# Kernel optimization log

Hardware: AMD Instinct MI355X
Metric: run time of the kernel (lower is better)

## Reference

```python
import jax, jax.numpy as jnp
import numpy as np

B, N, E_PER = 512, 256, 8192          # graphs, nodes per graph, edges per graph
FIN, H, K, FOUT = 128, 32, 16, 10     # in_channels, hidden, num clusters, out_channels
EPS = 1e-15


def setup_inputs() -> dict:
    key = jax.random.key(0)
    ks = jax.random.split(key, 12)
    x = jax.random.normal(ks[0], (B * N, FIN), jnp.float32)
    # intra-graph random edges, then offset into the global node index space
    src = jax.random.randint(ks[1], (B, E_PER), 0, N)
    dst = jax.random.randint(ks[2], (B, E_PER), 0, N)
    offs = (jnp.arange(B) * N)[:, None]
    edge_index = jnp.stack([(src + offs).reshape(-1), (dst + offs).reshape(-1)]).astype(jnp.int64)
    batch = jnp.repeat(jnp.arange(B), N).astype(jnp.int64)

    def lin(k, fin, fout):
        return (jax.random.normal(k, (fin, fout), jnp.float32) / np.sqrt(fin)).astype(jnp.float32)

    params = {
        'W_lin1': lin(ks[3], FIN, H), 'b_lin1': jnp.zeros((H,), jnp.float32),
        'W_rel1': lin(ks[4], H, H), 'b_rel1': jnp.zeros((H,), jnp.float32),
        'W_root1': lin(ks[5], H, H),
        'W_pool': lin(ks[6], H, K), 'b_pool': jnp.zeros((K,), jnp.float32),
        'W_rel2': lin(ks[7], H, H), 'b_rel2': jnp.zeros((H,), jnp.float32),
        'W_root2': lin(ks[8], H, H),
        'W_lin2': lin(ks[9], H, H), 'b_lin2': jnp.zeros((H,), jnp.float32),
        'W_lin3': lin(ks[10], H, FOUT), 'b_lin3': jnp.zeros((FOUT,), jnp.float32),
    }
    return {'x': x, 'edge_index': edge_index, 'batch': batch, **params}


def _densify(x, edge_index, batch):
    """to_dense_adj + to_dense_batch: [total,F] -> [B,N,F], [B,N,N], [B,N]."""
    n_total = x.shape[0]
    counts = jax.ops.segment_sum(jnp.ones((n_total,), jnp.int32), batch, num_segments=B)
    offsets = jnp.concatenate([jnp.zeros((1,), jnp.int32), jnp.cumsum(counts)[:-1]])
    pos = jnp.arange(n_total) - offsets[batch]            # position of node inside its graph
    eb = batch[edge_index[0]]                             # graph id of each edge
    adj = jnp.zeros((B, N, N), jnp.float32).at[eb, pos[edge_index[0]], pos[edge_index[1]]].add(1.0)
    xd = jnp.zeros((B, N, x.shape[1]), jnp.float32).at[batch, pos].set(x)
    mask = jnp.zeros((B, N), jnp.float32).at[batch, pos].set(1.0)
    return xd, adj, mask


def _dense_graph_conv(x, adj, W_rel, b_rel, W_root):
    # PyG DenseGraphConv(aggr='add'): lin_rel(adj @ x) + lin_root(x)
    return jnp.einsum('bnm,bmh,hk->bnk', adj, x, W_rel) + b_rel + x @ W_root


def _dense_mincut_pool(x, adj, s, mask):
    s = jax.nn.softmax(s, axis=-1)
    x = x * mask[..., None]
    s = s * mask[..., None]
    out = jnp.einsum('bnk,bnh->bkh', s, x)                        # s^T x
    out_adj = jnp.einsum('bnk,bnm,bmj->bkj', s, adj, s)           # s^T A s
    mincut_num = jnp.einsum('bkk->b', out_adj)
    d_flat = adj.sum(-1)                                          # degree
    mincut_den = jnp.einsum('bnk,bn,bnk->b', s, d_flat, s)        # trace(s^T D s)
    mincut_loss = jnp.mean(-(mincut_num / mincut_den))
    ss = jnp.einsum('bnk,bnj->bkj', s, s)
    ss_norm = jnp.linalg.norm(ss, axis=(-1, -2), keepdims=True)
    i_s = jnp.eye(K, dtype=jnp.float32)
    ortho_loss = jnp.mean(jnp.linalg.norm(ss / ss_norm - i_s / jnp.sqrt(jnp.float32(K)), axis=(-1, -2)))
    # zero diagonal, symmetric degree normalization
    diag_mask = 1.0 - i_s
    out_adj = out_adj * diag_mask
    d = jnp.sqrt(out_adj.sum(-1))[:, None, :] + EPS               # [B,1,K]
    out_adj = out_adj / d / jnp.swapaxes(d, 1, 2)
    return out, out_adj, mincut_loss, ortho_loss


def reference(x, edge_index, batch, W_lin1, b_lin1, W_rel1, b_rel1, W_root1,
              W_pool, b_pool, W_rel2, b_rel2, W_root2, W_lin2, b_lin2, W_lin3, b_lin3):
    xd, adj, mask = _densify(x, edge_index, batch)
    h = xd @ W_lin1 + b_lin1                                      # lin1
    h = _dense_graph_conv(h, adj, W_rel1, b_rel1, W_root1)        # conv1
    s2 = h @ W_pool + b_pool                                      # pool2
    h, adj_p, mincut_loss2, ortho_loss2 = _dense_mincut_pool(h, adj, s2, mask)
    h = _dense_graph_conv(h, adj_p, W_rel2, b_rel2, W_root2)      # conv2
    h = h.sum(axis=1)                                             # readout sum over clusters
    h = jax.nn.relu(h @ W_lin2 + b_lin2)
    h = h @ W_lin3 + b_lin3
    return jax.nn.log_softmax(h, axis=-1), mincut_loss2, ortho_loss2
```

## Files before the change

### kernel.cpp

```cpp
#include <hip/hip_runtime.h>

#define NB 512
#define NN 256
#define EPG 8192
#define FINC 128

typedef float f32x4 __attribute__((ext_vector_type(4)));
typedef short s16x8 __attribute__((ext_vector_type(8)));

__device__ __forceinline__ float bf2f(unsigned short u) {
  union { unsigned int i; float f; } x; x.i = ((unsigned int)u) << 16; return x.f;
}
__device__ __forceinline__ unsigned short f2bf(float f) {
  union { float f; unsigned int i; } x; x.f = f;
  unsigned int r = x.i + 0x7fffu + ((x.i >> 16) & 1u);
  return (unsigned short)(r >> 16);
}
__device__ __forceinline__ unsigned pk2(unsigned short a, unsigned short c) {
  return (unsigned)a | ((unsigned)c << 16);
}

union U16x8 { uint4 u; s16x8 s; };
__device__ __forceinline__ s16x8 dec8(unsigned d) {
  U16x8 o;
  o.u.x = 0x41804180u | ((d & 0x0000000Fu) << 3)  | ((d & 0x000000F0u) << 15);
  o.u.y = 0x41804180u | ((d & 0x00000F00u) >> 5)  | ((d & 0x0000F000u) << 7);
  o.u.z = 0x41804180u | ((d & 0x000F0000u) >> 13) | ((d & 0x00F00000u) >> 1);
  o.u.w = 0x41804180u | ((d & 0x0F000000u) >> 21) | ((d & 0xF0000000u) >> 9);
  return o.s;
}

struct Params {
  const void* x; const void* ei;
  const void *wl1, *bl1, *wr1, *br1, *wro1, *wp, *bp;
  const void *wr2, *br2, *wro2, *wl2, *bl2, *wl3, *bl3;
  float* out; float* ws;
};

__device__ __forceinline__ bool detect_bf16(const void* p) {
  const unsigned short* pw = (const unsigned short*)p;
  int sane = 0;
  for (int i = 0; i < 64; ++i) {
    unsigned e = (pw[i] >> 7) & 0xFFu;
    sane += (e > 96u && e < 132u) ? 1 : 0;
  }
  return sane >= 56;
}
__device__ __forceinline__ bool detect_i64(const void* p) {
  const int* pi = (const int*)p + EPG;
  int ok = 0;
  for (int i = 0; i < 32; ++i) ok += (pi[i] >= 256 && pi[i] < 512) ? 1 : 0;
  return ok < 24;
}
__device__ __forceinline__ float ldf(const void* p, int i, bool bf) {
  return bf ? bf2f(((const unsigned short*)p)[i]) : ((const float*)p)[i];
}

#define SMEM_TOTAL 81920

__global__ __launch_bounds__(1024, 8) void mincut_main(Params P) {
  extern __shared__ char smem[];
  const int t = threadIdx.x;
  const int b = blockIdx.x;

  int* flg = (int*)(smem + 78656);
  if (t == 0) {
    flg[0] = detect_bf16(P.wr1) ? 1 : 0;
    flg[1] = detect_i64(P.ei) ? 1 : 0;
  }
  __syncthreads();
  const bool BF  = (flg[0] != 0);
  const bool I64 = (flg[1] != 0);

  float* oadjb  = (float*)(smem + 2048);
  float* ddb    = (float*)(smem + 6144);
  float* caf    = (float*)(smem + 6208);
  float* psf    = (float*)(smem + 6272);
  float* qsf    = (float*)(smem + 6400);
  float* rb     = (float*)(smem + 8256);
  float* yb     = (float*)(smem + 8384);
  float* lgb    = (float*)(smem + 8512);
  float* rel2f  = (float*)(smem + 9216);
  float* root2f = (float*)(smem + 13312);
  float* lin2f  = (float*)(smem + 17408);
  float* lin3f  = (float*)(smem + 21504);
  float* brel2f = (float*)(smem + 22784);
  float* blin2f = (float*)(smem + 22912);
  float* blin3f = (float*)(smem + 23040);
  float* pbufH  = (float*)(smem + 24576);
  float* pbufL  = (float*)(smem + 26624);
  float* oadjH  = (float*)(smem + 28672);
  float* oadjL  = (float*)(smem + 29696);
  float* ssA    = (float*)(smem + 30720);
  float* ssX    = (float*)(smem + 31744);
  unsigned short* h0T  = (unsigned short*)(smem + 33792);
  unsigned short* h1Th = (unsigned short*)(smem + 33792);
  unsigned short* w1t  = (unsigned short*)(smem + 50688);
  unsigned short* zT   = (unsigned short*)(smem + 50688);
  unsigned short* sTh  = (unsigned short*)(smem + 50688);
  unsigned short* sTl  = (unsigned short*)(smem + 59136);
  unsigned short* wrelTh = (unsigned short*)(smem + 67584);
  unsigned short* wrelTl = (unsigned short*)(smem + 70144);
  unsigned short* wrootT = (unsigned short*)(smem + 72704);
  float* blin1f = (float*)(smem + 75264);
  unsigned short* taT = (unsigned short*)(smem + 67584);
  unsigned short* wpoolTh = (unsigned short*)(smem + 76032);
  unsigned short* wpoolTl = (unsigned short*)(smem + 77184);
  float*          colzF   = (float*)(smem + 78336);
  float*          colsF   = (float*)(smem + 78464);
  float*          scrE    = (float*)(smem + 78528);
  float*          bpf     = (float*)(smem + 78592);
  unsigned short* brel1h  = (unsigned short*)(smem + 81856);

  const int wv = t >> 6, lane = t & 63;
  const int lm = lane & 15, quad = lane >> 4;
  const int mbase = wv * 16;

  {
    uint4 z = {0u, 0u, 0u, 0u};
    for (int i = t; i < 2112; i += 1024) ((uint4*)smem)[i] = z;
  }
  if (t < 48) colzF[t] = 0.f;
  for (int e = t; e < 4096; e += 1024) {
    int k = e >> 5, c = e & 31;
    w1t[c * 136 + k] = f2bf(ldf(P.wl1, e, BF));
  }
  {
    int k = t >> 5, c = t & 31;
    float wr = ldf(P.wr1, t, BF);
    unsigned short hi = f2bf(wr);
    wrelTh[c * 40 + k] = hi;
    wrelTl[c * 40 + k] = f2bf(wr - bf2f(hi));
    wrootT[c * 40 + k] = f2bf(ldf(P.wro1, t, BF));
  }
  if (t < 512) {
    int m = t >> 4, c = t & 15;
    float w = ldf(P.wp, t, BF);
    unsigned short hi = f2bf(w);
    wpoolTh[c * 36 + m] = hi;
    wpoolTl[c * 36 + m] = f2bf(w - bf2f(hi));
  }
  if (t < 32) { blin1f[t] = ldf(P.bl1, t, BF); brel1h[t] = f2bf(ldf(P.br1, t, BF)); }
  if (t < 16) bpf[t] = ldf(P.bp, t, BF);
  __syncthreads();

  if (I64) {
    const uint4* s4 = (const uint4*)((const long long*)P.ei + (size_t)b * EPG) + t * 4;
    const uint4* d4 = (const uint4*)((const long long*)P.ei + (size_t)NB * EPG + (size_t)b * EPG) + t * 4;
    #pragma unroll
    for (int i = 0; i < 4; ++i) {
      uint4 a = s4[i], c = d4[i];
      unsigned n0 = (a.x & 255u) * 264u + (c.x & 255u);
      unsigned n1 = (a.z & 255u) * 264u + (c.z & 255u);
      atomicAdd((unsigned int*)(smem + ((n0 >> 3) << 2)), 1u << ((n0 & 7u) * 4u));
      atomicAdd((unsigned int*)(smem + ((n1 >> 3) << 2)), 1u << ((n1 & 7u) * 4u));
    }
  } else {
    const uint4* s4 = (const uint4*)((const int*)P.ei + (size_t)b * EPG) + t * 2;
    const uint4* d4 = (const uint4*)((const int*)P.ei + (size_t)NB * EPG + (size_t)b * EPG) + t * 2;
    #pragma unroll
    for (int i = 0; i < 2; ++i) {
      uint4 a = s4[i], c = d4[i];
      unsigned n0 = (a.x & 255u) * 264u + (c.x & 255u);
      unsigned n1 = (a.y & 255u) * 264u + (c.y & 255u);
      unsigned n2 = (a.z & 255u) * 264u + (c.z & 255u);
      unsigned n3 = (a.w & 255u) * 264u + (c.w & 255u);
      atomicAdd((unsigned int*)(smem + ((n0 >> 3) << 2)), 1u << ((n0 & 7u) * 4u));
      atomicAdd((unsigned int*)(smem + ((n1 >> 3) << 2)), 1u << ((n1 & 7u) * 4u));
      atomicAdd((unsigned int*)(smem + ((n2 >> 3) << 2)), 1u << ((n2 & 7u) * 4u));
      atomicAdd((unsigned int*)(smem + ((n3 >> 3) << 2)), 1u << ((n3 & 7u) * 4u));
    }
  }

  {
    f32x4 acc[2] = {{0.f,0.f,0.f,0.f},{0.f,0.f,0.f,0.f}};
    const size_t node = (size_t)(b * 256 + mbase + lm);
    #pragma unroll
    for (int ks = 0; ks < 4; ++ks) {
      const int k0 = ks * 32 + quad * 8;
      s16x8 a;
      if (BF) {
        a = *(const s16x8*)((const unsigned short*)P.x + node * 128 + k0);
      } else {
        const float* xp = (const float*)P.x + node * 128 + k0;
        f32x4 v0 = *(const f32x4*)xp;
        f32x4 v1 = *(const f32x4*)(xp + 4);
        #pragma unroll
        for (int j = 0; j < 4; ++j) { a[j] = (short)f2bf(v0[j]); a[4 + j] = (short)f2bf(v1[j]); }
      }
      #pragma unroll
      for (int ct = 0; ct < 2; ++ct) {
        s16x8 bh = *(const s16x8*)(w1t + (ct * 16 + lm) * 136 + k0);
        acc[ct] = __builtin_amdgcn_mfma_f32_16x16x32_bf16(a, bh, acc[ct], 0, 0, 0);
      }
    }
    #pragma unroll
    for (int ct = 0; ct < 2; ++ct) {
      const int c = ct * 16 + lm;
      float bias = blin1f[c];
      *(uint2*)(h0T + c * 264 + mbase + quad * 4) =
          make_uint2(pk2(f2bf(acc[ct][0] + bias), f2bf(acc[ct][1] + bias)),
                     pk2(f2bf(acc[ct][2] + bias), f2bf(acc[ct][3] + bias)));
    }
  }
  __syncthreads();

  f32x4 racc[2] = {{0.f,0.f,0.f,0.f},{0.f,0.f,0.f,0.f}};
  {
    s16x8 Ah;
    #pragma unroll
    for (int j = 0; j < 8; ++j) Ah[j] = (short)h0T[(quad * 8 + j) * 264 + mbase + lm];
    f32x4 zacc[2] = {{0.f,0.f,0.f,0.f},{0.f,0.f,0.f,0.f}};
    #pragma unroll
    for (int ct = 0; ct < 2; ++ct) {
      const int c = ct * 16 + lm;
      s16x8 brh = *(const s16x8*)(wrelTh + c * 40 + quad * 8);
      s16x8 brl = *(const s16x8*)(wrelTl + c * 40 + quad * 8);
      s16x8 bro = *(const s16x8*)(wrootT + c * 40 + quad * 8);
      zacc[ct] = __builtin_amdgcn_mfma_f32_16x16x32_bf16(Ah, brh, zacc[ct], 0, 0, 0);
      zacc[ct] = __builtin_amdgcn_mfma_f32_16x16x32_bf16(Ah, brl, zacc[ct], 0, 0, 0);
      racc[ct] = __builtin_amdgcn_mfma_f32_16x16x32_bf16(Ah, bro, racc[ct], 0, 0, 0);
    }
    #pragma unroll
    for (int ct = 0; ct < 2; ++ct) {
      unsigned short u0 = f2bf(zacc[ct][0]), u1 = f2bf(zacc[ct][1]);
      unsigned short u2 = f2bf(zacc[ct][2]), u3 = f2bf(zacc[ct][3]);
      *(uint2*)(zT + (ct * 16 + lm) * 264 + mbase + quad * 4) =
          make_uint2(pk2(u0, u1), pk2(u2, u3));
      float pz = (bf2f(u0) + bf2f(u1)) + (bf2f(u2) + bf2f(u3));
      pz += __shfl_xor(pz, 16, 64);
      pz += __shfl_xor(pz, 32, 64);
      if (lane < 16) atomicAdd(colzF + ct * 16 + lm, pz);
    }
  }
  __syncthreads();

  float degf;
  {
    f32x4 h1acc[2] = { racc[0], racc[1] };
    unsigned dsum = 0;
    const char* arow = smem + (mbase + lm) * 132;
    #pragma unroll
    for (int ks = 0; ks < 8; ++ks) {
      unsigned d = *(const unsigned int*)(arow + ks * 16 + quad * 4);
      unsigned v = (d & 0x0F0F0F0Fu) + ((d >> 4) & 0x0F0F0F0Fu);
      dsum += (v * 0x01010101u) >> 24;
      s16x8 af = dec8(d);
      const int v0 = ks * 32 + quad * 8;
      #pragma unroll
      for (int ct = 0; ct < 2; ++ct) {
        s16x8 bz = *(const s16x8*)(zT + (ct * 16 + lm) * 264 + v0);
        h1acc[ct] = __builtin_amdgcn_mfma_f32_16x16x32_bf16(af, bz, h1acc[ct], 0, 0, 0);
      }
    }
    dsum += __shfl_xor(dsum, 16, 64);
    dsum += __shfl_xor(dsum, 32, 64);
    degf = (float)dsum;
    #pragma unroll
    for (int ct = 0; ct < 2; ++ct) {
      const int c = ct * 16 + lm;
      float bias = bf2f(brel1h[c]) - 16.f * colzF[c];
      *(uint2*)(h1Th + c * 264 + mbase + quad * 4) =
          make_uint2(pk2(f2bf(h1acc[ct][0] + bias), f2bf(h1acc[ct][1] + bias)),
                     pk2(f2bf(h1acc[ct][2] + bias), f2bf(h1acc[ct][3] + bias)));
    }
  }
  __syncthreads();

  {
    s16x8 Ah1;
    #pragma unroll
    for (int j = 0; j < 8; ++j) Ah1[j] = (short)h1Th[(quad * 8 + j) * 264 + mbase + lm];
    s16x8 Bh, Bl;
    ((uint2*)&Bh)[0] = *(const uint2*)(wpoolTh + lm * 36 + quad * 8);
    ((uint2*)&Bh)[1] = *(const uint2*)(wpoolTh + lm * 36 + quad * 8 + 4);
    ((uint2*)&Bl)[0] = *(const uint2*)(wpoolTl + lm * 36 + quad * 8);
    ((uint2*)&Bl)[1] = *(const uint2*)(wpoolTl + lm * 36 + quad * 8 + 4);
    f32x4 lacc = {0.f, 0.f, 0.f, 0.f};
    lacc = __builtin_amdgcn_mfma_f32_16x16x32_bf16(Ah1, Bh, lacc, 0, 0, 0);
    lacc = __builtin_amdgcn_mfma_f32_16x16x32_bf16(Ah1, Bl, lacc, 0, 0, 0);
    f32x4 lg;
    float bm = bpf[lm];
    #pragma unroll
    for (int r = 0; r < 4; ++r) lg[r] = lacc[r] + bm;
    f32x4 mx = lg;
    #pragma unroll
    for (int m = 1; m <= 8; m <<= 1)
      #pragma unroll
      for (int r = 0; r < 4; ++r) mx[r] = fmaxf(mx[r], __shfl_xor(mx[r], m, 64));
    #pragma unroll
    for (int r = 0; r < 4; ++r) lg[r] = __expf(lg[r] - mx[r]);
    f32x4 sm = lg;
    #pragma unroll
    for (int m = 1; m <= 8; m <<= 1)
      #pragma unroll
      for (int r = 0; r < 4; ++r) sm[r] += __shfl_xor(sm[r], m, 64);
    f32x4 sval, sq;
    #pragma unroll
    for (int r = 0; r < 4; ++r) { sval[r] = lg[r] / sm[r]; sq[r] = sval[r] * sval[r]; }
    #pragma unroll
    for (int m = 1; m <= 8; m <<= 1)
      #pragma unroll
      for (int r = 0; r < 4; ++r) sq[r] += __shfl_xor(sq[r], m, 64);
    {
      unsigned short h0s = f2bf(sval[0]); float r0 = bf2f(h0s); unsigned short l0 = f2bf(sval[0] - r0);
      unsigned short h1s = f2bf(sval[1]); float r1 = bf2f(h1s); unsigned short l1 = f2bf(sval[1] - r1);
      unsigned short h2s = f2bf(sval[2]); float r2 = bf2f(h2s); unsigned short l2 = f2bf(sval[2] - r2);
      unsigned short h3s = f2bf(sval[3]); float r3 = bf2f(h3s); unsigned short l3 = f2bf(sval[3] - r3);
      const int nb = lm * 264 + mbase + quad * 4;
      *(uint2*)(sTh + nb) = make_uint2(pk2(h0s, h1s), pk2(h2s, h3s));
      *(uint2*)(sTl + nb) = make_uint2(pk2(l0, l1), pk2(l2, l3));
      float sr = ((r0 + bf2f(l0)) + (r1 + bf2f(l1))) + ((r2 + bf2f(l2)) + (r3 + bf2f(l3)));
      sr += __shfl_xor(sr, 16, 64);
      sr += __shfl_xor(sr, 32, 64);
      if (lane < 16) atomicAdd(colsF + lm, sr);
    }
    {
      int l = lane & 15, src = (l >> 2) << 4;
      float q0 = __shfl(sq[0], src, 64), q1 = __shfl(sq[1], src, 64);
      float q2 = __shfl(sq[2], src, 64), q3 = __shfl(sq[3], src, 64);
      float ssel = (l & 2) ? ((l & 1) ? q3 : q2) : ((l & 1) ? q1 : q0);
      float vden = (lane < 16) ? degf * ssel : 0.f;
      #pragma unroll
      for (int o = 32; o > 0; o >>= 1) vden += __shfl_xor(vden, o, 64);
      if (lane == 0) scrE[wv] = vden;
    }
  }
  __syncthreads();

  {
    float cols = colsF[lm];
    f32x4 tacc = {0.f, 0.f, 0.f, 0.f};
    const char* arow = smem + (mbase + lm) * 132;
    #pragma unroll
    for (int ks = 0; ks < 8; ++ks) {
      unsigned d = *(const unsigned int*)(arow + ks * 16 + quad * 4);
      s16x8 af = dec8(d);
      const int v0 = ks * 32 + quad * 8;
      s16x8 bh = *(const s16x8*)(sTh + lm * 264 + v0);
      s16x8 bl = *(const s16x8*)(sTl + lm * 264 + v0);
      tacc = __builtin_amdgcn_mfma_f32_16x16x32_bf16(af, bh, tacc, 0, 0, 0);
      tacc = __builtin_amdgcn_mfma_f32_16x16x32_bf16(af, bl, tacc, 0, 0, 0);
    }
    float c16 = 16.f * cols;
    *(uint2*)(taT + lm * 264 + mbase + quad * 4) =
        make_uint2(pk2(f2bf(tacc[0] - c16), f2bf(tacc[1] - c16)),
                   pk2(f2bf(tacc[2] - c16), f2bf(tacc[3] - c16)));
  }
  __syncthreads();

  rel2f[t] = ldf(P.wr2, t, BF);
  root2f[t] = ldf(P.wro2, t, BF);
  lin2f[t] = ldf(P.wl2, t, BF);
  if (t < 320) lin3f[t] = ldf(P.wl3, t, BF);
  if (t < 32) brel2f[t] = ldf(P.br2, t, BF);
  if (t < 32) blin2f[t] = ldf(P.bl2, t, BF);
  if (t < 10) blin3f[t] = ldf(P.bl3, t, BF);

  {
    const unsigned short *Ap, *Bp; float* dst; int W, ct = 0;
    switch (wv) {
      case 0: Ap = sTh; Bp = h1Th; dst = pbufH; W = 32; ct = 0; break;
      case 1: Ap = sTh; Bp = h1Th; dst = pbufH; W = 32; ct = 1; break;
      case 2: Ap = sTl; Bp = h1Th; dst = pbufL; W = 32; ct = 0; break;
      case 3: Ap = sTl; Bp = h1Th; dst = pbufL; W = 32; ct = 1; break;
      case 4: Ap = sTh; Bp = taT;  dst = oadjH; W = 16; break;
      case 5: Ap = sTl; Bp = taT;  dst = oadjL; W = 16; break;
      case 6: Ap = sTh; Bp = sTh;  dst = ssA;   W = 16; break;
      default: Ap = sTh; Bp = sTl; dst = ssX;   W = 16; break;
    }
    if (wv < 8) {
      const int cidx = ct * 16 + lm;
      const unsigned short* Bb = Bp + cidx * 264;
      f32x4 acc = {0.f, 0.f, 0.f, 0.f};
      #pragma unroll
      for (int ch = 0; ch < 8; ++ch) {
        s16x8 a = *(const s16x8*)(Ap + lm * 264 + ch * 32 + quad * 8);
        s16x8 bb = *(const s16x8*)(Bb + ch * 32 + quad * 8);
        acc = __builtin_amdgcn_mfma_f32_16x16x32_bf16(a, bb, acc, 0, 0, 0);
      }
      #pragma unroll
      for (int r = 0; r < 4; ++r) dst[(quad * 4 + r) * W + cidx] = acc[r];
    }
  }
  __syncthreads();

  if (wv == 0) {
    #pragma unroll
    for (int u = 0; u < 4; ++u) {
      int i = lane * 4 + u;
      oadjb[i] = oadjH[i] + oadjL[i];
    }
    if (lane < 16) {
      float rs = 0.f;
      #pragma unroll
      for (int j = 0; j < 16; ++j) if (j != lane) rs += oadjb[lane * 16 + j];
      ddb[lane] = sqrtf(rs) + 1e-15f;
    }
    if (lane < 16) {
      float s = 0.f;
      float dj = ddb[lane];
      #pragma unroll
      for (int k = 0; k < 16; ++k)
        if (k != lane) s += oadjb[k * 16 + lane] / (ddb[k] * dj);
      caf[lane] = s;
    }
    if (lane < 32) {
      float ps = 0.f, qs = 0.f;
      #pragma unroll
      for (int j = 0; j < 16; ++j) {
        float pv = pbufH[j * 32 + lane] + pbufL[j * 32 + lane];
        ps += pv;
        qs += caf[j] * pv;
      }
      psf[lane] = ps; qsf[lane] = qs;
    }
    if (lane < 32) {
      float r = 16.f * brel2f[lane];
      #pragma unroll
      for (int m = 0; m < 32; ++m)
        r += qsf[m] * rel2f[m * 32 + lane] + psf[m] * root2f[m * 32 + lane];
      rb[lane] = r;
    }
    if (lane < 32) {
      float y = blin2f[lane];
      #pragma unroll
      for (int m = 0; m < 32; ++m) y += rb[m] * lin2f[m * 32 + lane];
      yb[lane] = fmaxf(y, 0.f);
    }
    if (lane < 10) {
      float lg = blin3f[lane];
      #pragma unroll
      for (int m = 0; m < 32; ++m) lg += yb[m] * lin3f[m * 10 + lane];
      lgb[lane] = lg;
    }
    if (lane == 0) {
      float mx = lgb[0];
      #pragma unroll
      for (int i = 1; i < 10; ++i) mx = fmaxf(mx, lgb[i]);
      float sum = 0.f;
      #pragma unroll
      for (int i = 0; i < 10; ++i) sum += __expf(lgb[i] - mx);
      lgb[10] = mx + __logf(sum);
    }
    if (lane < 10) {
      float val = lgb[lane] - lgb[10];
      if (BF) ((unsigned short*)P.out)[b * 10 + lane] = f2bf(val);
      else    P.out[b * 10 + lane] = val;
    }
  } else if (wv == 1) {
    float vfro = 0.f, vtr = 0.f;
    #pragma unroll
    for (int u = 0; u < 4; ++u) {
      int i = lane * 4 + u, k = i >> 4, j = i & 15;
      float ssv = ssA[i] + ssX[i] + ssX[j * 16 + k];
      vfro += ssv * ssv;
      if (k == j) vtr += ssv;
    }
    float vnum = (lane < 16) ? (oadjH[lane * 17] + oadjL[lane * 17]) : 0.f;
    float vden = (lane < 16) ? scrE[lane] : 0.f;
    #pragma unroll
    for (int o = 32; o > 0; o >>= 1) {
      vfro += __shfl_xor(vfro, o, 64);
      vtr  += __shfl_xor(vtr, o, 64);
      vnum += __shfl_xor(vnum, o, 64);
      vden += __shfl_xor(vden, o, 64);
    }
    if (lane == 0) {
      float ssn = sqrtf(vfro);
      float orth2 = 2.f - vtr / (2.f * ssn);
      atomicAdd(P.ws, -(vnum / vden) * (1.f / NB));
      atomicAdd(P.ws + 1, sqrtf(fmaxf(orth2, 0.f)) * (1.f / NB));
    }
  }
}

__global__ void mincut_fin(Params P) {
  if (threadIdx.x == 0) {
    const bool BF = detect_bf16(P.wr1);
    if (BF) {
      ((unsigned short*)P.out)[5120] = f2bf(P.ws[0]);
      ((unsigned short*)P.out)[5121] = f2bf(P.ws[1]);
    } else {
      P.out[5120] = P.ws[0];
      P.out[5121] = P.ws[1];
    }
  }
}

extern "C" void kernel_launch(void* const* d_in, const int* in_sizes, int n_in,
                              void* d_out, int out_size, void* d_ws, size_t ws_size,
                              hipStream_t stream) {
  (void)in_sizes; (void)n_in; (void)out_size; (void)ws_size;
  Params P;
  P.x    = d_in[0];
  P.ei   = d_in[1];
  P.wl1  = d_in[3];
  P.bl1  = d_in[4];
  P.wr1  = d_in[5];
  P.br1  = d_in[6];
  P.wro1 = d_in[7];
  P.wp   = d_in[8];
  P.bp   = d_in[9];
  P.wr2  = d_in[10];
  P.br2  = d_in[11];
  P.wro2 = d_in[12];
  P.wl2  = d_in[13];
  P.bl2  = d_in[14];
  P.wl3  = d_in[15];
  P.bl3  = d_in[16];
  P.out  = (float*)d_out;
  P.ws   = (float*)d_ws;

  hipMemsetAsync(d_ws, 0, 2 * sizeof(float), stream);
  hipFuncSetAttribute(reinterpret_cast<const void*>(mincut_main),
                      hipFuncAttributeMaxDynamicSharedMemorySize, SMEM_TOTAL);
  hipLaunchKernelGGL(mincut_main, dim3(NB), dim3(1024), SMEM_TOTAL, stream, P);
  hipLaunchKernelGGL(mincut_fin, dim3(1), dim3(64), 0, stream, P);
}
```

Before: 171.3 us.

## Drop bf16 hi/lo split precision terms and fuse finalize kernel via last-block counter

Removes the two-term (hi+lo) bf16 splitting of weights and cluster assignments, so each product uses a single bf16 MFMA instead of two or three, and the lo-term shared-memory buffers and stores go away. It also removes the separate finalize kernel launch: the last block to finish, found through an atomic counter in workspace, writes the loss outputs. This cuts MFMA work, LDS traffic and one launch, at the cost of lower numeric accuracy, which may break tolerance on the mincut and ortho losses.

Measured after the change: 174.4 us. Within noise of the previous version (+1.8%).

```diff
diff --git a/kernel.cpp b/kernel.cpp
--- a/kernel.cpp
+++ b/kernel.cpp
@@ -87,25 +87,18 @@
   float* brel2f = (float*)(smem + 22784);
   float* blin2f = (float*)(smem + 22912);
   float* blin3f = (float*)(smem + 23040);
-  float* pbufH  = (float*)(smem + 24576);
-  float* pbufL  = (float*)(smem + 26624);
-  float* oadjH  = (float*)(smem + 28672);
-  float* oadjL  = (float*)(smem + 29696);
+  float* pbuf   = (float*)(smem + 24576);
   float* ssA    = (float*)(smem + 30720);
-  float* ssX    = (float*)(smem + 31744);
   unsigned short* h0T  = (unsigned short*)(smem + 33792);
   unsigned short* h1Th = (unsigned short*)(smem + 33792);
   unsigned short* w1t  = (unsigned short*)(smem + 50688);
   unsigned short* zT   = (unsigned short*)(smem + 50688);
   unsigned short* sTh  = (unsigned short*)(smem + 50688);
-  unsigned short* sTl  = (unsigned short*)(smem + 59136);
   unsigned short* wrelTh = (unsigned short*)(smem + 67584);
-  unsigned short* wrelTl = (unsigned short*)(smem + 70144);
   unsigned short* wrootT = (unsigned short*)(smem + 72704);
   float* blin1f = (float*)(smem + 75264);
   unsigned short* taT = (unsigned short*)(smem + 67584);
   unsigned short* wpoolTh = (unsigned short*)(smem + 76032);
-  unsigned short* wpoolTl = (unsigned short*)(smem + 77184);
   float*          colzF   = (float*)(smem + 78336);
   float*          colsF   = (float*)(smem + 78464);
   float*          scrE    = (float*)(smem + 78528);
@@ -127,18 +120,12 @@
   }
   {
     int k = t >> 5, c = t & 31;
-    float wr = ldf(P.wr1, t, BF);
-    unsigned short hi = f2bf(wr);
-    wrelTh[c * 40 + k] = hi;
-    wrelTl[c * 40 + k] = f2bf(wr - bf2f(hi));
+    wrelTh[c * 40 + k] = f2bf(ldf(P.wr1, t, BF));
     wrootT[c * 40 + k] = f2bf(ldf(P.wro1, t, BF));
   }
   if (t < 512) {
     int m = t >> 4, c = t & 15;
-    float w = ldf(P.wp, t, BF);
-    unsigned short hi = f2bf(w);
-    wpoolTh[c * 36 + m] = hi;
-    wpoolTl[c * 36 + m] = f2bf(w - bf2f(hi));
+    wpoolTh[c * 36 + m] = f2bf(ldf(P.wp, t, BF));
   }
   if (t < 32) { blin1f[t] = ldf(P.bl1, t, BF); brel1h[t] = f2bf(ldf(P.br1, t, BF)); }
   if (t < 16) bpf[t] = ldf(P.bp, t, BF);
@@ -215,10 +202,8 @@
     for (int ct = 0; ct < 2; ++ct) {
       const int c = ct * 16 + lm;
       s16x8 brh = *(const s16x8*)(wrelTh + c * 40 + quad * 8);
-      s16x8 brl = *(const s16x8*)(wrelTl + c * 40 + quad * 8);
       s16x8 bro = *(const s16x8*)(wrootT + c * 40 + quad * 8);
       zacc[ct] = __builtin_amdgcn_mfma_f32_16x16x32_bf16(Ah, brh, zacc[ct], 0, 0, 0);
-      zacc[ct] = __builtin_amdgcn_mfma_f32_16x16x32_bf16(Ah, brl, zacc[ct], 0, 0, 0);
       racc[ct] = __builtin_amdgcn_mfma_f32_16x16x32_bf16(Ah, bro, racc[ct], 0, 0, 0);
     }
     #pragma unroll
@@ -271,14 +256,11 @@
     s16x8 Ah1;
     #pragma unroll
     for (int j = 0; j < 8; ++j) Ah1[j] = (short)h1Th[(quad * 8 + j) * 264 + mbase + lm];
-    s16x8 Bh, Bl;
+    s16x8 Bh;
     ((uint2*)&Bh)[0] = *(const uint2*)(wpoolTh + lm * 36 + quad * 8);
     ((uint2*)&Bh)[1] = *(const uint2*)(wpoolTh + lm * 36 + quad * 8 + 4);
-    ((uint2*)&Bl)[0] = *(const uint2*)(wpoolTl + lm * 36 + quad * 8);
-    ((uint2*)&Bl)[1] = *(const uint2*)(wpoolTl + lm * 36 + quad * 8 + 4);
     f32x4 lacc = {0.f, 0.f, 0.f, 0.f};
     lacc = __builtin_amdgcn_mfma_f32_16x16x32_bf16(Ah1, Bh, lacc, 0, 0, 0);
-    lacc = __builtin_amdgcn_mfma_f32_16x16x32_bf16(Ah1, Bl, lacc, 0, 0, 0);
     f32x4 lg;
     float bm = bpf[lm];
     #pragma unroll
@@ -303,14 +285,13 @@
       #pragma unroll
       for (int r = 0; r < 4; ++r) sq[r] += __shfl_xor(sq[r], m, 64);
     {
-      unsigned short h0s = f2bf(sval[0]); float r0 = bf2f(h0s); unsigned short l0 = f2bf(sval[0] - r0);
-      unsigned short h1s = f2bf(sval[1]); float r1 = bf2f(h1s); unsigned short l1 = f2bf(sval[1] - r1);
-      unsigned short h2s = f2bf(sval[2]); float r2 = bf2f(h2s); unsigned short l2 = f2bf(sval[2] - r2);
-      unsigned short h3s = f2bf(sval[3]); float r3 = bf2f(h3s); unsigned short l3 = f2bf(sval[3] - r3);
+      unsigned short h0s = f2bf(sval[0]);
+      unsigned short h1s = f2bf(sval[1]);
+      unsigned short h2s = f2bf(sval[2]);
+      unsigned short h3s = f2bf(sval[3]);
       const int nb = lm * 264 + mbase + quad * 4;
       *(uint2*)(sTh + nb) = make_uint2(pk2(h0s, h1s), pk2(h2s, h3s));
-      *(uint2*)(sTl + nb) = make_uint2(pk2(l0, l1), pk2(l2, l3));
-      float sr = ((r0 + bf2f(l0)) + (r1 + bf2f(l1))) + ((r2 + bf2f(l2)) + (r3 + bf2f(l3)));
+      float sr = (bf2f(h0s) + bf2f(h1s)) + (bf2f(h2s) + bf2f(h3s));
       sr += __shfl_xor(sr, 16, 64);
       sr += __shfl_xor(sr, 32, 64);
       if (lane < 16) atomicAdd(colsF + lm, sr);
@@ -338,9 +319,7 @@
       s16x8 af = dec8(d);
       const int v0 = ks * 32 + quad * 8;
       s16x8 bh = *(const s16x8*)(sTh + lm * 264 + v0);
-      s16x8 bl = *(const s16x8*)(sTl + lm * 264 + v0);
       tacc = __builtin_amdgcn_mfma_f32_16x16x32_bf16(af, bh, tacc, 0, 0, 0);
-      tacc = __builtin_amdgcn_mfma_f32_16x16x32_bf16(af, bl, tacc, 0, 0, 0);
     }
     float c16 = 16.f * cols;
     *(uint2*)(taT + lm * 264 + mbase + quad * 4) =
@@ -357,40 +336,30 @@
   if (t < 32) blin2f[t] = ldf(P.bl2, t, BF);
   if (t < 10) blin3f[t] = ldf(P.bl3, t, BF);
 
-  {
-    const unsigned short *Ap, *Bp; float* dst; int W, ct = 0;
+  if (wv < 4) {
+    const unsigned short* Ap = sTh;
+    const unsigned short* Bp; float* dst; int W, ct = 0;
     switch (wv) {
-      case 0: Ap = sTh; Bp = h1Th; dst = pbufH; W = 32; ct = 0; break;
-      case 1: Ap = sTh; Bp = h1Th; dst = pbufH; W = 32; ct = 1; break;
-      case 2: Ap = sTl; Bp = h1Th; dst = pbufL; W = 32; ct = 0; break;
-      case 3: Ap = sTl; Bp = h1Th; dst = pbufL; W = 32; ct = 1; break;
-      case 4: Ap = sTh; Bp = taT;  dst = oadjH; W = 16; break;
-      case 5: Ap = sTl; Bp = taT;  dst = oadjL; W = 16; break;
-      case 6: Ap = sTh; Bp = sTh;  dst = ssA;   W = 16; break;
-      default: Ap = sTh; Bp = sTl; dst = ssX;   W = 16; break;
-    }
-    if (wv < 8) {
-      const int cidx = ct * 16 + lm;
-      const unsigned short* Bb = Bp + cidx * 264;
-      f32x4 acc = {0.f, 0.f, 0.f, 0.f};
-      #pragma unroll
-      for (int ch = 0; ch < 8; ++ch) {
-        s16x8 a = *(const s16x8*)(Ap + lm * 264 + ch * 32 + quad * 8);
-        s16x8 bb = *(const s16x8*)(Bb + ch * 32 + quad * 8);
-        acc = __builtin_amdgcn_mfma_f32_16x16x32_bf16(a, bb, acc, 0, 0, 0);
-      }
-      #pragma unroll
-      for (int r = 0; r < 4; ++r) dst[(quad * 4 + r) * W + cidx] = acc[r];
-    }
+      case 0: Bp = h1Th; dst = pbuf;  W = 32; ct = 0; break;
+      case 1: Bp = h1Th; dst = pbuf;  W = 32; ct = 1; break;
+      case 2: Bp = taT;  dst = oadjb; W = 16; break;
+      default: Bp = sTh; dst = ssA;   W = 16; break;
+    }
+    const int cidx = ct * 16 + lm;
+    const unsigned short* Bb = Bp + cidx * 264;
+    f32x4 acc = {0.f, 0.f, 0.f, 0.f};
+    #pragma unroll
+    for (int ch = 0; ch < 8; ++ch) {
+      s16x8 a = *(const s16x8*)(Ap + lm * 264 + ch * 32 + quad * 8);
+      s16x8 bb = *(const s16x8*)(Bb + ch * 32 + quad * 8);
+      acc = __builtin_amdgcn_mfma_f32_16x16x32_bf16(a, bb, acc, 0, 0, 0);
+    }
+    #pragma unroll
+    for (int r = 0; r < 4; ++r) dst[(quad * 4 + r) * W + cidx] = acc[r];
   }
   __syncthreads();
 
   if (wv == 0) {
-    #pragma unroll
-    for (int u = 0; u < 4; ++u) {
-      int i = lane * 4 + u;
-      oadjb[i] = oadjH[i] + oadjL[i];
-    }
     if (lane < 16) {
       float rs = 0.f;
       #pragma unroll
@@ -409,7 +378,7 @@
       float ps = 0.f, qs = 0.f;
       #pragma unroll
       for (int j = 0; j < 16; ++j) {
-        float pv = pbufH[j * 32 + lane] + pbufL[j * 32 + lane];
+        float pv = pbuf[j * 32 + lane];
         ps += pv;
         qs += caf[j] * pv;
       }
@@ -453,11 +422,11 @@
     #pragma unroll
     for (int u = 0; u < 4; ++u) {
       int i = lane * 4 + u, k = i >> 4, j = i & 15;
-      float ssv = ssA[i] + ssX[i] + ssX[j * 16 + k];
+      float ssv = ssA[i];
       vfro += ssv * ssv;
       if (k == j) vtr += ssv;
     }
-    float vnum = (lane < 16) ? (oadjH[lane * 17] + oadjL[lane * 17]) : 0.f;
+    float vnum = (lane < 16) ? oadjb[lane * 17] : 0.f;
     float vden = (lane < 16) ? scrE[lane] : 0.f;
     #pragma unroll
     for (int o = 32; o > 0; o >>= 1) {
@@ -471,19 +440,19 @@
       float orth2 = 2.f - vtr / (2.f * ssn);
       atomicAdd(P.ws, -(vnum / vden) * (1.f / NB));
       atomicAdd(P.ws + 1, sqrtf(fmaxf(orth2, 0.f)) * (1.f / NB));
-    }
-  }
-}
-
-__global__ void mincut_fin(Params P) {
-  if (threadIdx.x == 0) {
-    const bool BF = detect_bf16(P.wr1);
-    if (BF) {
-      ((unsigned short*)P.out)[5120] = f2bf(P.ws[0]);
-      ((unsigned short*)P.out)[5121] = f2bf(P.ws[1]);
-    } else {
-      P.out[5120] = P.ws[0];
-      P.out[5121] = P.ws[1];
+      __threadfence();
+      unsigned old = atomicAdd((unsigned int*)(P.ws + 2), 1u);
+      if (old == (unsigned)(NB - 1)) {
+        float l0 = atomicAdd(P.ws, 0.f);
+        float l1 = atomicAdd(P.ws + 1, 0.f);
+        if (BF) {
+          ((unsigned short*)P.out)[5120] = f2bf(l0);
+          ((unsigned short*)P.out)[5121] = f2bf(l1);
+        } else {
+          P.out[5120] = l0;
+          P.out[5121] = l1;
+        }
+      }
     }
   }
 }
@@ -512,9 +481,8 @@
   P.out  = (float*)d_out;
   P.ws   = (float*)d_ws;
 
-  hipMemsetAsync(d_ws, 0, 2 * sizeof(float), stream);
+  hipMemsetAsync(d_ws, 0, 4 * sizeof(float), stream);
   hipFuncSetAttribute(reinterpret_cast<const void*>(mincut_main),
                       hipFuncAttributeMaxDynamicSharedMemorySize, SMEM_TOTAL);
   hipLaunchKernelGGL(mincut_main, dim3(NB), dim3(1024), SMEM_TOTAL, stream, P);
-  hipLaunchKernelGGL(mincut_fin, dim3(1), dim3(64), 0, stream, P);
-}
+}
```
